# Kernel optimization log

Measured on AMD Instinct MI355X. Metric: run time of the kernel, lower is better.

Reference implementation:

```python
import jax, jax.numpy as jnp
import numpy as np

NUM_PTS = 8   # num_points_per_face
K = 5         # self.k


def _sq_dist(x, y):
    # squared euclidean distance matrix (Nx, Ny); matches torch.cdist**2 / sum((a-b)**2)
    x2 = jnp.sum(x * x, axis=1)[:, None]
    y2 = jnp.sum(y * y, axis=1)[None, :]
    d = x2 + y2 - 2.0 * (x @ y.T)
    return jnp.maximum(d, 0.0)


def setup_inputs() -> dict:
    key = jax.random.key(0)
    k1, k2, k3, k4, k5, k6, k7 = jax.random.split(key, 7)
    V, Fs, Ft = 2048, 4096, 4096
    return {
        "source_vertices": jax.random.normal(k1, (1, V, 3), dtype=jnp.float32),
        "source_faces": jax.random.randint(k2, (Fs, 3), 0, V),
        "target_vertices": jax.random.normal(k3, (1, V, 3), dtype=jnp.float32),
        "target_faces": jax.random.randint(k4, (3, Ft), 0, V),
        "face_probs": jax.random.uniform(k5, (Fs,), dtype=jnp.float32),
        "r1u": jax.random.uniform(k6, (Fs, NUM_PTS), dtype=jnp.float32),
        "r2u": jax.random.uniform(k7, (Fs, NUM_PTS), dtype=jnp.float32),
    }


def reference(source_vertices, source_faces, target_vertices, target_faces, face_probs, r1u, r2u):
    sv = source_vertices[0]                 # (V, 3)
    tv = target_vertices[0]                 # (V, 3)
    tf = target_faces.T                     # (Ft, 3)
    Fs = source_faces.shape[0]

    src_bc = sv[source_faces].mean(axis=1)  # (Fs, 3) source barycenters
    tgt_bc = tv[tf].mean(axis=1)            # (Ft, 3) target barycenters

    # ---- forward loss: prob-weighted min squared distance to target barycenters
    d_fwd = _sq_dist(src_bc, tgt_bc)        # (Fs, Ft)
    forward_loss = jnp.sum(face_probs * jnp.min(d_fwd, axis=1))

    # ---- sample points from triangles via barycentric coords
    r1 = jnp.sqrt(r1u)
    w1 = 1.0 - r1
    w2 = r1 * (1.0 - r2u)
    w3 = r1 * r2u
    v1 = sv[source_faces[:, 0]]             # (Fs, 3)
    v2 = sv[source_faces[:, 1]]
    v3 = sv[source_faces[:, 2]]
    pts = (w1[..., None] * v1[:, None] + w2[..., None] * v2[:, None]
           + w3[..., None] * v3[:, None]).reshape(-1, 3)   # (P, 3), P = Fs*NUM_PTS
    pt_faces = jnp.repeat(jnp.arange(Fs), NUM_PTS)          # (P,)
    pt_probs = face_probs[pt_faces]                         # (P,)

    # ---- reverse loss, batched over all P points
    d_src = _sq_dist(pts, src_bc)                           # (P, Fs)
    neg_d, idx = jax.lax.top_k(-d_src, K + 1)               # K+1 smallest distances
    tri_dists = -neg_d                                      # (P, K+1)
    mask = idx != pt_faces[:, None]                         # exclude own face
    has_self = jnp.any(~mask, axis=1)
    excl_pos = jnp.where(has_self, jnp.argmin(mask, axis=1), K + 1)  # (P,)
    t = jnp.arange(K)
    sel = t[None, :] + (t[None, :] >= excl_pos[:, None]).astype(jnp.int32)  # (P, K)
    valid_dists = jnp.take_along_axis(tri_dists, sel, axis=1)   # (P, K)
    valid_idx = jnp.take_along_axis(idx, sel, axis=1)           # (P, K)
    valid_probs = face_probs[valid_idx]                         # (P, K)

    min_tgt = jnp.min(_sq_dist(pts, tgt_bc), axis=1)            # (P,)

    reverse_loss = jnp.sum(pt_probs * min_tgt
                           + (1.0 - pt_probs) * jnp.mean(valid_probs * valid_dists, axis=1))
    return forward_loss + reverse_loss
```

## Files before the change

kernel.cpp:

```cpp
#include <hip/hip_runtime.h>
#include <math.h>

#define FS 4096
#define FT 4096
#define TS 1024
#define BIGF 3.0e38f
#define KEYINF 0xFFFFFFFFu

typedef float v2f __attribute__((ext_vector_type(2)));

__device__ __forceinline__ unsigned umin32(unsigned a, unsigned b) { return a < b ? a : b; }
__device__ __forceinline__ unsigned umax32(unsigned a, unsigned b) { return a < b ? b : a; }

__device__ __forceinline__ unsigned med3u(unsigned a, unsigned b, unsigned c) {
    unsigned d;
    asm("v_med3_u32 %0, %1, %2, %3" : "=v"(d) : "v"(a), "v"(b), "v"(c));
    return d;
}

__device__ __forceinline__ v2f pk_fma(v2f a, v2f b, v2f c) {
    v2f d;
    asm("v_pk_fma_f32 %0, %1, %2, %3" : "=v"(d) : "v"(a), "v"(b), "v"(c));
    return d;
}
__device__ __forceinline__ v2f pk_add(v2f a, v2f b) {
    v2f d;
    asm("v_pk_add_f32 %0, %1, %2" : "=v"(d) : "v"(a), "v"(b));
    return d;
}

__device__ __forceinline__ float block_reduce_sum(float v) {
    __shared__ float s[8];
    for (int o = 32; o > 0; o >>= 1) v += __shfl_down(v, o, 64);
    int lane = threadIdx.x & 63, wid = threadIdx.x >> 6;
    if (lane == 0) s[wid] = v;
    __syncthreads();
    int nw = blockDim.x >> 6;
    v = (threadIdx.x < (unsigned)nw) ? s[threadIdx.x] : 0.f;
    if (wid == 0)
        for (int o = 4; o > 0; o >>= 1) v += __shfl_down(v, o, 64);
    return v;
}

#define CE(x, y) { unsigned _n = umin32(x, y); y = umax32(x, y); x = _n; }

__device__ __forceinline__ void merge32(unsigned s[6]) {
    #pragma unroll
    for (int m = 1; m <= 16; m <<= 1) {
        unsigned b0 = __shfl_xor(s[0], m, 64), b1 = __shfl_xor(s[1], m, 64);
        unsigned b2 = __shfl_xor(s[2], m, 64), b3 = __shfl_xor(s[3], m, 64);
        unsigned b4 = __shfl_xor(s[4], m, 64), b5 = __shfl_xor(s[5], m, 64);
        unsigned l0 = s[0], l1 = s[1];
        unsigned l2 = umin32(s[2], b5), l3 = umin32(s[3], b4);
        unsigned l4 = umin32(s[4], b3), l5 = umin32(s[5], b2);
        unsigned l6 = b1, l7 = b0;
        CE(l0, l4) CE(l1, l5) CE(l2, l6) CE(l3, l7)
        CE(l0, l2) CE(l1, l3) CE(l4, l6) CE(l5, l7)
        CE(l0, l1) CE(l2, l3) CE(l4, l5) CE(l6, l7)
        s[0] = l0; s[1] = l1; s[2] = l2; s[3] = l3; s[4] = l4; s[5] = l5;
    }
}

__global__ __launch_bounds__(64) void k_prep(
        const float* __restrict__ sv, const int* __restrict__ sf,
        const float* __restrict__ tv, const int* __restrict__ tf,
        float4* __restrict__ sbc2, float4* __restrict__ tbc2,
        float4* __restrict__ sbcr, float* __restrict__ out) {
    int i = blockIdx.x * 64 + threadIdx.x;
    if (i == 0) out[0] = 0.f;
    if (i >= FS) return;
    const float third = 1.f / 3.f;
    int a = sf[3*i], b = sf[3*i+1], c = sf[3*i+2];
    float x = (sv[3*a  ] + sv[3*b  ] + sv[3*c  ]) * third;
    float y = (sv[3*a+1] + sv[3*b+1] + sv[3*c+1]) * third;
    float z = (sv[3*a+2] + sv[3*b+2] + sv[3*c+2]) * third;
    float n2 = x*x + y*y + z*z;
    sbcr[i] = make_float4(x, y, z, n2);
    int ta = tf[i], tb = tf[FT + i], tc = tf[2*FT + i];
    float tx = (tv[3*ta  ] + tv[3*tb  ] + tv[3*tc  ]) * third;
    float ty = (tv[3*ta+1] + tv[3*tb+1] + tv[3*tc+1]) * third;
    float tz = (tv[3*ta+2] + tv[3*tb+2] + tv[3*tc+2]) * third;
    float tn2 = tx*tx + ty*ty + tz*tz;

    int tt = i >> 10, cc = i & 1023;
    int g = cc >> 6, half = (cc >> 5) & 1, pp = cc & 31;
    int lo4 = tt*1024 + g*32 + pp, hi4 = lo4 + 512;
    float* S = (float*)sbc2;
    S[4*lo4 + half]     = -2.f*x;  S[4*lo4 + 2 + half] = -2.f*y;
    S[4*hi4 + half]     = -2.f*z;  S[4*hi4 + 2 + half] = n2;
    float* T = (float*)tbc2;
    T[4*lo4 + half]     = -2.f*tx; T[4*lo4 + 2 + half] = -2.f*ty;
    T[4*hi4 + half]     = -2.f*tz; T[4*hi4 + 2 + half] = tn2;
}

__global__ __launch_bounds__(256, 4) void k_main(
        const float* __restrict__ sv, const int* __restrict__ sf,
        const float* __restrict__ fp,
        const float* __restrict__ r1u, const float* __restrict__ r2u,
        const float4* __restrict__ sbc2, const float4* __restrict__ tbc2,
        const float4* __restrict__ sbcr, float* __restrict__ out) {
    __shared__ float4 tileS[TS];
    __shared__ float4 tileT[TS];
    int tid  = threadIdx.x;
    int seg  = tid & 31;
    int slot = tid >> 5;
    float contrib = 0.f;

    if (blockIdx.x < 1024) {
        int pt0  = blockIdx.x * 32 + slot * 4;
        int face = pt0 >> 3;

        int a = sf[3*face], b = sf[3*face+1], c = sf[3*face+2];
        float ax = sv[3*a], ay = sv[3*a+1], az = sv[3*a+2];
        float bx = sv[3*b], by = sv[3*b+1], bz = sv[3*b+2];
        float cx = sv[3*c], cy = sv[3*c+1], cz = sv[3*c+2];
        float4 r14 = ((const float4*)r1u)[pt0 >> 2];
        float4 r24 = ((const float4*)r2u)[pt0 >> 2];
        float p2s[4];
        v2f pxb[4], pyb[4], pzb[4], p2b[4];
        {
            float r1a[4] = {r14.x, r14.y, r14.z, r14.w};
            float r2a[4] = {r24.x, r24.y, r24.z, r24.w};
            #pragma unroll
            for (int i = 0; i < 4; ++i) {
                float r1 = sqrtf(r1a[i]);
                float w1 = 1.f - r1, w2 = r1 * (1.f - r2a[i]), w3 = r1 * r2a[i];
                float px = w1*ax + w2*bx + w3*cx;
                float py = w1*ay + w2*by + w3*cy;
                float pz = w1*az + w2*bz + w3*cz;
                float p2 = px*px + py*py + pz*pz;
                p2s[i] = p2;
                pxb[i] = (v2f){px, px}; pyb[i] = (v2f){py, py};
                pzb[i] = (v2f){pz, pz}; p2b[i] = (v2f){p2, p2};
            }
        }

        unsigned s0[4], s1[4], s2[4];
        #pragma unroll
        for (int i = 0; i < 4; ++i) { s0[i]=KEYINF; s1[i]=KEYINF; s2[i]=KEYINF; }
        v2f vm2[4];
        #pragma unroll
        for (int i = 0; i < 4; ++i) vm2[i] = (v2f){BIGF, BIGF};

        for (int p = 0; p < 4; ++p) {
            int t0 = p * TS;
            #pragma unroll
            for (int j = 0; j < 4; ++j) {
                tileS[tid + j*256] = sbc2[t0 + tid + j*256];
                tileT[tid + j*256] = tbc2[t0 + tid + j*256];
            }
            __syncthreads();
            unsigned jja = (unsigned)(t0 + seg);
            #pragma unroll 4
            for (int jp = 0; jp < 16; ++jp) {
                float4 lo = tileS[(jp << 5) + seg];
                float4 hi = tileS[512 + (jp << 5) + seg];
                v2f cx2 = {lo.x, lo.y}, cy2 = {lo.z, lo.w};
                v2f cz2 = {hi.x, hi.y}, cw2 = {hi.z, hi.w};
                #pragma unroll
                for (int i = 0; i < 4; ++i) {
                    v2f d2 = pk_add(cw2, p2b[i]);
                    d2 = pk_fma(pzb[i], cz2, d2);
                    d2 = pk_fma(pyb[i], cy2, d2);
                    d2 = pk_fma(pxb[i], cx2, d2);
                    unsigned ka = (__float_as_uint(d2.x) & 0xFFFFF000u) | jja;
                    unsigned kb = (__float_as_uint(d2.y) & 0xFFFFF000u) | (jja + 32u);
                    unsigned n0 = umin32(s0[i], ka);
                    unsigned n1 = med3u(s0[i], s1[i], ka);
                    unsigned n2 = med3u(s1[i], s2[i], ka);
                    s0[i]=n0; s1[i]=n1; s2[i]=n2;
                    n0 = umin32(s0[i], kb);
                    n1 = med3u(s0[i], s1[i], kb);
                    n2 = med3u(s1[i], s2[i], kb);
                    s0[i]=n0; s1[i]=n1; s2[i]=n2;
                }
                jja += 64;
            }
            #pragma unroll 4
            for (int jp = 0; jp < 16; ++jp) {
                float4 lo = tileT[(jp << 5) + seg];
                float4 hi = tileT[512 + (jp << 5) + seg];
                v2f cx2 = {lo.x, lo.y}, cy2 = {lo.z, lo.w};
                v2f cz2 = {hi.x, hi.y}, cw2 = {hi.z, hi.w};
                #pragma unroll
                for (int i = 0; i < 4; ++i) {
                    v2f t = pk_fma(pzb[i], cz2, cw2);
                    t = pk_fma(pyb[i], cy2, t);
                    t = pk_fma(pxb[i], cx2, t);
                    vm2[i].x = fminf(vm2[i].x, t.x);
                    vm2[i].y = fminf(vm2[i].y, t.y);
                }
            }
            __syncthreads();
        }

        float vm[4];
        #pragma unroll
        for (int i = 0; i < 4; ++i) {
            float v = fminf(vm2[i].x, vm2[i].y);
            v = fminf(v, __shfl_xor(v, 1, 64));
            v = fminf(v, __shfl_xor(v, 2, 64));
            v = fminf(v, __shfl_xor(v, 4, 64));
            v = fminf(v, __shfl_xor(v, 8, 64));
            v = fminf(v, __shfl_xor(v, 16, 64));
            vm[i] = v;
        }

        float pf = fp[face];
        float csum = 0.f;
        #pragma unroll
        for (int i = 0; i < 4; ++i) {
            unsigned srt[6] = {s0[i], s1[i], s2[i], KEYINF, KEYINF, KEYINF};
            merge32(srt);
            if (seg == 0) {
                int   q0 = srt[0] & 0xFFF, q1 = srt[1] & 0xFFF, q2 = srt[2] & 0xFFF;
                int   q3 = srt[3] & 0xFFF, q4 = srt[4] & 0xFFF, q5 = srt[5] & 0xFFF;
                float d0 = __uint_as_float(srt[0] & 0xFFFFF000u);
                float d1 = __uint_as_float(srt[1] & 0xFFFFF000u);
                float d2 = __uint_as_float(srt[2] & 0xFFFFF000u);
                float d3 = __uint_as_float(srt[3] & 0xFFFFF000u);
                float d4 = __uint_as_float(srt[4] & 0xFFFFF000u);
                float d5 = __uint_as_float(srt[5] & 0xFFFFF000u);

                int skip = 5;
                if      (q0 == face) skip = 0;
                else if (q1 == face) skip = 1;
                else if (q2 == face) skip = 2;
                else if (q3 == face) skip = 3;
                else if (q4 == face) skip = 4;

                float s = 0.f;
                if (skip != 0) s += fp[q0] * d0;
                if (skip != 1) s += fp[q1] * d1;
                if (skip != 2) s += fp[q2] * d2;
                if (skip != 3) s += fp[q3] * d3;
                if (skip != 4) s += fp[q4] * d4;
                if (skip != 5) s += fp[q5] * d5;

                float mtd = fmaxf(vm[i] + p2s[i], 0.f);
                csum += pf * mtd + (1.f - pf) * (s * 0.2f);
            }
        }
        if (seg == 0) contrib = csum;
    } else {
        int f0 = (blockIdx.x - 1024) * 32 + slot * 4;
        float qw[4];
        v2f qxb[4], qyb[4], qzb[4];
        #pragma unroll
        for (int i = 0; i < 4; ++i) {
            float4 q = sbcr[f0 + i];
            qxb[i] = (v2f){q.x, q.x}; qyb[i] = (v2f){q.y, q.y};
            qzb[i] = (v2f){q.z, q.z}; qw[i] = q.w;
        }
        v2f vf2[4];
        #pragma unroll
        for (int i = 0; i < 4; ++i) vf2[i] = (v2f){BIGF, BIGF};

        for (int p = 0; p < 4; ++p) {
            int t0 = p * TS;
            #pragma unroll
            for (int j = 0; j < 4; ++j) tileT[tid + j*256] = tbc2[t0 + tid + j*256];
            __syncthreads();
            #pragma unroll 4
            for (int jp = 0; jp < 16; ++jp) {
                float4 lo = tileT[(jp << 5) + seg];
                float4 hi = tileT[512 + (jp << 5) + seg];
                v2f cx2 = {lo.x, lo.y}, cy2 = {lo.z, lo.w};
                v2f cz2 = {hi.x, hi.y}, cw2 = {hi.z, hi.w};
                #pragma unroll
                for (int i = 0; i < 4; ++i) {
                    v2f t = pk_fma(qzb[i], cz2, cw2);
                    t = pk_fma(qyb[i], cy2, t);
                    t = pk_fma(qxb[i], cx2, t);
                    vf2[i].x = fminf(vf2[i].x, t.x);
                    vf2[i].y = fminf(vf2[i].y, t.y);
                }
            }
            __syncthreads();
        }
        float vf[4];
        #pragma unroll
        for (int i = 0; i < 4; ++i) {
            float v = fminf(vf2[i].x, vf2[i].y);
            v = fminf(v, __shfl_xor(v, 1, 64));
            v = fminf(v, __shfl_xor(v, 2, 64));
            v = fminf(v, __shfl_xor(v, 4, 64));
            v = fminf(v, __shfl_xor(v, 8, 64));
            v = fminf(v, __shfl_xor(v, 16, 64));
            vf[i] = v;
        }
        if (seg == 0)
            contrib = fp[f0  ] * fmaxf(vf[0] + qw[0], 0.f)
                    + fp[f0+1] * fmaxf(vf[1] + qw[1], 0.f)
                    + fp[f0+2] * fmaxf(vf[2] + qw[2], 0.f)
                    + fp[f0+3] * fmaxf(vf[3] + qw[3], 0.f);
    }

    float tot = block_reduce_sum(contrib);
    if (tid == 0) atomicAdd(out, tot);
}

extern "C" void kernel_launch(void* const* d_in, const int* in_sizes, int n_in,
                              void* d_out, int out_size, void* d_ws, size_t ws_size,
                              hipStream_t stream) {
    const float* sv  = (const float*)d_in[0];
    const int*   sf  = (const int*)  d_in[1];
    const float* tv  = (const float*)d_in[2];
    const int*   tf  = (const int*)  d_in[3];
    const float* fp  = (const float*)d_in[4];
    const float* r1u = (const float*)d_in[5];
    const float* r2u = (const float*)d_in[6];
    float* out = (float*)d_out;

    char* ws = (char*)d_ws;
    float4* sbc2 = (float4*)(ws);
    float4* tbc2 = (float4*)(ws + 65536);
    float4* sbcr = (float4*)(ws + 131072);

    k_prep<<<64,   64,  0, stream>>>(sv, sf, tv, tf, sbc2, tbc2, sbcr, out);
    k_main<<<1152, 256, 0, stream>>>(sv, sf, fp, r1u, r2u, sbc2, tbc2, sbcr, out);
}
```

Measured before the change: 114.4 us.

## Load tiles via global_load_lds, halve LDS tile size, raise occupancy

Halves the LDS tile from 1024 to 512 float4 entries and loops over eight phases instead of four. Tiles are now loaded with direct global-to-LDS transfers, which bypass VGPR staging. Launch bounds are raised to 8 blocks per CU so more waves can hide latency, which puts pressure on the register budget. The phase indexing is remapped so each half-tile keeps the lo/hi packed layout, and the trailing barrier is moved to the top of the loop.

```diff
diff --git a/kernel.cpp b/kernel.cpp
--- a/kernel.cpp
+++ b/kernel.cpp
@@ -3,7 +3,8 @@
 
 #define FS 4096
 #define FT 4096
-#define TS 1024
+#define TS 512
+#define NPH 8
 #define BIGF 3.0e38f
 #define KEYINF 0xFFFFFFFFu
 
@@ -27,6 +28,12 @@
     v2f d;
     asm("v_pk_add_f32 %0, %1, %2" : "=v"(d) : "v"(a), "v"(b));
     return d;
+}
+
+__device__ __forceinline__ void gl_lds16(const float4* g, float4* l) {
+    __builtin_amdgcn_global_load_lds(
+        (__attribute__((address_space(1))) void*)(g),
+        (__attribute__((address_space(3))) void*)(l), 16, 0, 0);
 }
 
 __device__ __forceinline__ float block_reduce_sum(float v) {
@@ -93,7 +100,7 @@
     T[4*hi4 + half]     = -2.f*tz; T[4*hi4 + 2 + half] = tn2;
 }
 
-__global__ __launch_bounds__(256, 4) void k_main(
+__global__ __launch_bounds__(256, 8) void k_main(
         const float* __restrict__ sv, const int* __restrict__ sf,
         const float* __restrict__ fp,
         const float* __restrict__ r1u, const float* __restrict__ r2u,
@@ -116,7 +123,6 @@
         float cx = sv[3*c], cy = sv[3*c+1], cz = sv[3*c+2];
         float4 r14 = ((const float4*)r1u)[pt0 >> 2];
         float4 r24 = ((const float4*)r2u)[pt0 >> 2];
-        float p2s[4];
         v2f pxb[4], pyb[4], pzb[4], p2b[4];
         {
             float r1a[4] = {r14.x, r14.y, r14.z, r14.w};
@@ -129,7 +135,6 @@
                 float py = w1*ay + w2*by + w3*cy;
                 float pz = w1*az + w2*bz + w3*cz;
                 float p2 = px*px + py*py + pz*pz;
-                p2s[i] = p2;
                 pxb[i] = (v2f){px, px}; pyb[i] = (v2f){py, py};
                 pzb[i] = (v2f){pz, pz}; p2b[i] = (v2f){p2, p2};
             }
@@ -142,19 +147,19 @@
         #pragma unroll
         for (int i = 0; i < 4; ++i) vm2[i] = (v2f){BIGF, BIGF};
 
-        for (int p = 0; p < 4; ++p) {
-            int t0 = p * TS;
-            #pragma unroll
-            for (int j = 0; j < 4; ++j) {
-                tileS[tid + j*256] = sbc2[t0 + tid + j*256];
-                tileT[tid + j*256] = tbc2[t0 + tid + j*256];
-            }
+        for (int p = 0; p < NPH; ++p) {
+            int loB = ((p >> 1) << 10) + ((p & 1) << 8);
             __syncthreads();
-            unsigned jja = (unsigned)(t0 + seg);
+            gl_lds16(&sbc2[loB + tid],       &tileS[tid]);
+            gl_lds16(&sbc2[loB + 512 + tid], &tileS[256 + tid]);
+            gl_lds16(&tbc2[loB + tid],       &tileT[tid]);
+            gl_lds16(&tbc2[loB + 512 + tid], &tileT[256 + tid]);
+            __syncthreads();
+            unsigned jja = (unsigned)(p * TS + seg);
             #pragma unroll 4
-            for (int jp = 0; jp < 16; ++jp) {
+            for (int jp = 0; jp < 8; ++jp) {
                 float4 lo = tileS[(jp << 5) + seg];
-                float4 hi = tileS[512 + (jp << 5) + seg];
+                float4 hi = tileS[256 + (jp << 5) + seg];
                 v2f cx2 = {lo.x, lo.y}, cy2 = {lo.z, lo.w};
                 v2f cz2 = {hi.x, hi.y}, cw2 = {hi.z, hi.w};
                 #pragma unroll
@@ -177,9 +182,9 @@
                 jja += 64;
             }
             #pragma unroll 4
-            for (int jp = 0; jp < 16; ++jp) {
+            for (int jp = 0; jp < 8; ++jp) {
                 float4 lo = tileT[(jp << 5) + seg];
-                float4 hi = tileT[512 + (jp << 5) + seg];
+                float4 hi = tileT[256 + (jp << 5) + seg];
                 v2f cx2 = {lo.x, lo.y}, cy2 = {lo.z, lo.w};
                 v2f cz2 = {hi.x, hi.y}, cw2 = {hi.z, hi.w};
                 #pragma unroll
@@ -191,7 +196,6 @@
                     vm2[i].y = fminf(vm2[i].y, t.y);
                 }
             }
-            __syncthreads();
         }
 
         float vm[4];
@@ -237,7 +241,7 @@
                 if (skip != 4) s += fp[q4] * d4;
                 if (skip != 5) s += fp[q5] * d5;
 
-                float mtd = fmaxf(vm[i] + p2s[i], 0.f);
+                float mtd = fmaxf(vm[i] + p2b[i].x, 0.f);
                 csum += pf * mtd + (1.f - pf) * (s * 0.2f);
             }
         }
@@ -256,15 +260,16 @@
         #pragma unroll
         for (int i = 0; i < 4; ++i) vf2[i] = (v2f){BIGF, BIGF};
 
-        for (int p = 0; p < 4; ++p) {
-            int t0 = p * TS;
-            #pragma unroll
-            for (int j = 0; j < 4; ++j) tileT[tid + j*256] = tbc2[t0 + tid + j*256];
+        for (int p = 0; p < NPH; ++p) {
+            int loB = ((p >> 1) << 10) + ((p & 1) << 8);
+            __syncthreads();
+            gl_lds16(&tbc2[loB + tid],       &tileT[tid]);
+            gl_lds16(&tbc2[loB + 512 + tid], &tileT[256 + tid]);
             __syncthreads();
             #pragma unroll 4
-            for (int jp = 0; jp < 16; ++jp) {
+            for (int jp = 0; jp < 8; ++jp) {
                 float4 lo = tileT[(jp << 5) + seg];
-                float4 hi = tileT[512 + (jp << 5) + seg];
+                float4 hi = tileT[256 + (jp << 5) + seg];
                 v2f cx2 = {lo.x, lo.y}, cy2 = {lo.z, lo.w};
                 v2f cz2 = {hi.x, hi.y}, cw2 = {hi.z, hi.w};
                 #pragma unroll
@@ -276,7 +281,6 @@
                     vf2[i].y = fminf(vf2[i].y, t.y);
                 }
             }
-            __syncthreads();
         }
         float vf[4];
         #pragma unroll
```

New measurement: 129.2 us. +12.9%, slower.
